# Optimization experiments

Measured on AMD Instinct MI355X. Metric: run time of the kernel, lower is better.

The kernel has to match this reference:

```python
import jax, jax.numpy as jnp
import numpy as np

NUM_CLASSES = 2
THRESHOLD = 0.35
NEGPOS_RATIO = 7
VARIANCES = (0.1, 0.2)
B, P, O = 64, 16800, 64  # batch, num_priors, num_objs per image


def point_form(pr):
    # cxcywh -> xyxy
    return jnp.concatenate([pr[:, :2] - pr[:, 2:] / 2, pr[:, :2] + pr[:, 2:] / 2], axis=1)


def jaccard(a, b):
    # a: [A,4] xyxy, b: [Bx,4] xyxy -> IoU [A,Bx]
    lt = jnp.maximum(a[:, None, :2], b[None, :, :2])
    rb = jnp.minimum(a[:, None, 2:], b[None, :, 2:])
    wh = jnp.clip(rb - lt, 0.0)
    inter = wh[..., 0] * wh[..., 1]
    area_a = ((a[:, 2] - a[:, 0]) * (a[:, 3] - a[:, 1]))[:, None]
    area_b = ((b[:, 2] - b[:, 0]) * (b[:, 3] - b[:, 1]))[None, :]
    return inter / (area_a + area_b - inter)


def encode(matched, priors):
    # matched xyxy [P,4], priors cxcywh [P,4]
    g_cxcy = (matched[:, :2] + matched[:, 2:]) / 2 - priors[:, :2]
    g_cxcy = g_cxcy / (VARIANCES[0] * priors[:, 2:])
    g_wh = (matched[:, 2:] - matched[:, :2]) / priors[:, 2:]
    g_wh = jnp.log(g_wh) / VARIANCES[1]
    return jnp.concatenate([g_cxcy, g_wh], axis=1)


def encode_landm(matched, priors):
    # matched [P,10] -> [P,5,2]
    m = matched.reshape(-1, 5, 2)
    g = (m - priors[:, None, :2]) / (VARIANCES[0] * priors[:, None, 2:])
    return g.reshape(-1, 10)


def match_one(truths, labels, landms, priors):
    # truths [O,4], labels [O], landms [O,10]
    overlaps = jaccard(truths, point_form(priors))  # [O,P]
    best_prior_overlap = overlaps.max(axis=1)       # per-gt best IoU
    best_prior_idx = overlaps.argmax(axis=1)
    valid_gt = best_prior_overlap >= 0.2
    best_truth_overlap = overlaps.max(axis=0)       # per-prior best IoU
    best_truth_idx = overlaps.argmax(axis=0)
    # index_fill(2) only for valid gts (best_prior_idx_filter)
    bto = best_truth_overlap.at[best_prior_idx].set(
        jnp.where(valid_gt, 2.0, best_truth_overlap[best_prior_idx]))
    # ensure every gt keeps its best prior
    bti = best_truth_idx.at[best_prior_idx].set(jnp.arange(truths.shape[0]))
    matches = truths[bti]                  # [P,4]
    conf = labels[bti]                     # [P]
    conf = jnp.where(bto < THRESHOLD, 0.0, conf)
    loc = encode(matches, priors)
    landm = encode_landm(landms[bti], priors)
    return loc, conf, landm


def smooth_l1_sum(x, mask):
    ax = jnp.abs(x)
    v = jnp.where(ax < 1.0, 0.5 * ax * ax, ax - 0.5)
    return (v * mask).sum()


def setup_inputs() -> dict:
    key = jax.random.key(0)
    k1, k2, k3, k4, k5, k6, k7, k8 = jax.random.split(key, 8)
    loc_data = jax.random.normal(k1, (B, P, 4), jnp.float32)
    conf_data = jax.random.normal(k2, (B, P, NUM_CLASSES), jnp.float32)
    landm_data = jax.random.normal(k3, (B, P, 10), jnp.float32)
    # priors: cx,cy in (0,1), w,h in (0.02,0.22)
    cxy = jax.random.uniform(k4, (P, 2), jnp.float32)
    wh = jax.random.uniform(k5, (P, 2), jnp.float32) * 0.2 + 0.02
    priors = jnp.concatenate([cxy, wh], axis=1)
    # targets: valid corner boxes + landmarks + label in {1,-1}
    xy1 = jax.random.uniform(k6, (B, O, 2), jnp.float32) * 0.6
    bwh = jax.random.uniform(k7, (B, O, 2), jnp.float32) * 0.3 + 0.05
    boxes = jnp.concatenate([xy1, xy1 + bwh], axis=-1)
    lms = jax.random.uniform(k8, (B, O, 10), jnp.float32)
    lab = jnp.where(jax.random.uniform(jax.random.fold_in(key, 9), (B, O, 1)) < 0.3, -1.0, 1.0)
    targets = jnp.concatenate([boxes, lms, lab], axis=-1)
    return {"loc_data": loc_data, "conf_data": conf_data, "landm_data": landm_data,
            "priors": priors, "targets": targets}


def reference(loc_data, conf_data, landm_data, priors, targets):
    num = loc_data.shape[0]
    num_priors = priors.shape[0]
    truths = targets[:, :, :4]
    landms = targets[:, :, 4:14]
    labels = targets[:, :, -1]
    loc_t, conf_t, landm_t = jax.vmap(match_one, in_axes=(0, 0, 0, None))(
        truths, labels, landms, priors)  # [B,P,4], [B,P], [B,P,10]

    # landmark loss over conf_t > 0
    pos1 = conf_t > 0
    num_pos_landm = pos1.astype(jnp.int32).sum(axis=1, keepdims=True)
    N1 = jnp.maximum(num_pos_landm.sum().astype(jnp.float32), 1.0)
    loss_landm = smooth_l1_sum(landm_data - landm_t, pos1[..., None].astype(landm_data.dtype))

    # localization loss over conf_t != 0 ; conf_t[pos] = 1
    pos = conf_t != 0
    conf_t01 = jnp.where(pos, 1, 0)  # int {0,1}
    loss_l = smooth_l1_sum(loc_data - loc_t, pos[..., None].astype(loc_data.dtype))

    # hard negative mining on per-prior CE loss (global-max log_sum_exp, as in source)
    batch_conf = conf_data.reshape(-1, NUM_CLASSES)
    x_max = batch_conf.max()
    lse = jnp.log(jnp.exp(batch_conf - x_max).sum(axis=1, keepdims=True)) + x_max
    gathered = jnp.take_along_axis(batch_conf, conf_t01.reshape(-1, 1), axis=1)
    loss_c = (lse - gathered).reshape(num, -1)  # [B,P]; positives NOT zeroed (as in source)
    loss_idx = jnp.argsort(-loss_c, axis=1)
    idx_rank = jnp.argsort(loss_idx, axis=1)
    num_pos = pos.astype(jnp.int32).sum(axis=1, keepdims=True)  # [B,1]
    num_neg = jnp.minimum(NEGPOS_RATIO * num_pos, num_priors - 1)
    neg = idx_rank < num_neg  # [B,P]
    neg_pos = pos | neg

    # cross-entropy (sum) over selected pos+neg priors
    logp = jax.nn.log_softmax(conf_data, axis=-1)  # [B,P,C]
    ce = -jnp.take_along_axis(logp, conf_t01[..., None], axis=-1)[..., 0]
    loss_c_final = (ce * neg_pos.astype(ce.dtype)).sum()

    N = jnp.maximum(num_pos.sum().astype(jnp.float32), 1.0)
    return (loss_l / N, loss_c_final / N, loss_landm / N1)
```

## Files before the change

kernel.cpp:

```cpp
#include <hip/hip_runtime.h>
#include <math.h>

#define BN 64
#define PN 16800
#define ON 64
#define THRESH 0.35f
#define NEGPOS 7
#define GX 66
#define NBLK (BN * GX)
#define NBP 1024
#define NCELL 256
#define NCB 66
#define EPSW 0.0009765625f
#define IOUF 0.3499f
#define TAILT 104

__device__ __forceinline__ unsigned f2key(float f) {
  unsigned u = __float_as_uint(f);
  return (u & 0x80000000u) ? ~u : (u | 0x80000000u);
}
__device__ __forceinline__ float key2f(unsigned k) {
  unsigned u = (k & 0x80000000u) ? (k & 0x7FFFFFFFu) : ~k;
  return __uint_as_float(u);
}
__device__ __forceinline__ float sl1(float d) {
  float a = fabsf(d);
  return (a < 1.f) ? 0.5f * a * a : a - 0.5f;
}

__global__ void k_count(const float* __restrict__ priors,
                        unsigned char* __restrict__ pcell,
                        unsigned* __restrict__ gcnt,
                        unsigned* __restrict__ gmax) {
  __shared__ unsigned lcnt[NCELL];
  int tid = threadIdx.x;
  lcnt[tid] = 0;
  __syncthreads();
  int p = blockIdx.x * 256 + tid;
  float mw = 0.f, mh = 0.f;
  if (p < PN) {
    float4 pr = reinterpret_cast<const float4*>(priors)[p];
    int cx = (int)(pr.x * 16.f); cx = cx < 0 ? 0 : (cx > 15 ? 15 : cx);
    int cy = (int)(pr.y * 16.f); cy = cy < 0 ? 0 : (cy > 15 ? 15 : cy);
    int cell = cy * 16 + cx;
    pcell[p] = (unsigned char)cell;
    atomicAdd(&lcnt[cell], 1u);
    mw = pr.z * 0.5f;
    mh = pr.w * 0.5f;
  }
#pragma unroll
  for (int off = 32; off; off >>= 1) {
    mw = fmaxf(mw, __shfl_xor(mw, off));
    mh = fmaxf(mh, __shfl_xor(mh, off));
  }
  if ((tid & 63) == 0) {
    atomicMax(&gmax[0], __float_as_uint(mw));
    atomicMax(&gmax[1], __float_as_uint(mh));
  }
  __syncthreads();
  unsigned c = lcnt[tid];
  if (c) atomicAdd(&gcnt[tid], c);
}

__global__ void k_scatter(const float* __restrict__ priors,
                          const float* __restrict__ targets,
                          const unsigned char* __restrict__ pcell,
                          const unsigned* __restrict__ gcnt,
                          unsigned* __restrict__ gcur,
                          const unsigned* __restrict__ gmax,
                          float4* __restrict__ sbox,
                          int* __restrict__ sorig,
                          int* __restrict__ cellOff,
                          unsigned long long* __restrict__ tmask) {
  int bid = blockIdx.x;
  int tid = threadIdx.x;
  if (bid < NCB) {
    __shared__ unsigned tmp[NCELL];
    __shared__ unsigned excl[NCELL];
    __shared__ unsigned lcnt[NCELL];
    __shared__ unsigned lbase[NCELL];
    unsigned c = gcnt[tid];
    tmp[tid] = c;
    lcnt[tid] = 0;
    __syncthreads();
    for (int off = 1; off < NCELL; off <<= 1) {
      unsigned v = (tid >= off) ? tmp[tid - off] : 0u;
      __syncthreads();
      tmp[tid] += v;
      __syncthreads();
    }
    excl[tid] = tmp[tid] - c;
    if (bid == 0) {
      cellOff[tid] = (int)(tmp[tid] - c);
      if (tid == 0) cellOff[NCELL] = PN;
    }
    __syncthreads();
    int p = bid * 256 + tid;
    bool valid = p < PN;
    int cell = 0; unsigned lrank = 0;
    if (valid) {
      cell = pcell[p];
      lrank = atomicAdd(&lcnt[cell], 1u);
    }
    __syncthreads();
    if (lcnt[tid]) lbase[tid] = atomicAdd(&gcur[tid], lcnt[tid]);
    __syncthreads();
    if (valid) {
      int slot = (int)(excl[cell] + lbase[cell] + lrank);
      float4 pr = reinterpret_cast<const float4*>(priors)[p];
      float px1 = pr.x - pr.z * 0.5f, py1 = pr.y - pr.w * 0.5f;
      float px2 = pr.x + pr.z * 0.5f, py2 = pr.y + pr.w * 0.5f;
      sbox[slot] = make_float4(px1, py1, px2, py2);
      sorig[slot] = p;
    }
  } else {
    int b = bid - NCB;
    __shared__ float4 tb[ON];
    if (tid < ON) {
      const float* tg = &targets[((long)b * ON + tid) * 15];
      tb[tid] = make_float4(tg[0], tg[1], tg[2], tg[3]);
    }
    __syncthreads();
    float MW = __uint_as_float(gmax[0]), MH = __uint_as_float(gmax[1]);
    int cx = tid & 15, cy = tid >> 4;
    float cxl = (float)cx * 0.0625f, cxh = (float)(cx + 1) * 0.0625f;
    float cyl = (float)cy * 0.0625f, cyh = (float)(cy + 1) * 0.0625f;
    float pmaxa = 4.f * MW * MH;
    unsigned long long m = 0ull;
    for (int t = 0; t < ON; t++) {
      float4 a = tb[t];
      float wt = a.z - a.x, ht = a.w - a.y;
      float at = wt * ht;
      float need = IOUF * at;
      float wmin = need / fminf(ht, 2.f * MH);
      float hmin = need / fminf(wt, 2.f * MW);
      float wx0 = a.x + wmin - MW - EPSW, wx1 = a.z - wmin + MW + EPSW;
      float wy0 = a.y + hmin - MH - EPSW, wy1 = a.w - hmin + MH + EPSW;
      bool ok = (pmaxa >= need) &&
                (cxh > wx0) && (cxl < wx1) &&
                (cyh > wy0) && (cyl < wy1);
      if (ok) m |= (1ull << t);
    }
    tmask[b * NCELL + tid] = m;
  }
}

__global__ void k_bp(const float* __restrict__ targets,
                     const float4* __restrict__ sbox,
                     const int* __restrict__ sorig,
                     const int* __restrict__ cellOff,
                     const unsigned* __restrict__ gmax,
                     unsigned long long* __restrict__ bpp) {
  int bid = blockIdx.x;
  int tid = threadIdx.x;
  int lane = tid & 63, wv = tid >> 6;
  int b = bid >> 4;
  int t = ((bid & 15) << 2) + wv;
  const float* tg = &targets[((long)b * ON + t) * 15];
  float ax1 = tg[0], ay1 = tg[1], ax2 = tg[2], ay2 = tg[3];
  float aa = (ax2 - ax1) * (ay2 - ay1);
  float MW = __uint_as_float(gmax[0]), MH = __uint_as_float(gmax[1]);
  int xlo = (int)floorf((ax1 - MW - EPSW) * 16.f); xlo = xlo < 0 ? 0 : (xlo > 15 ? 15 : xlo);
  int xhi = (int)floorf((ax2 + MW + EPSW) * 16.f); xhi = xhi < 0 ? 0 : (xhi > 15 ? 15 : xhi);
  int ylo = (int)floorf((ay1 - MH - EPSW) * 16.f); ylo = ylo < 0 ? 0 : (ylo > 15 ? 15 : ylo);
  int yhi = (int)floorf((ay2 + MH + EPSW) * 16.f); yhi = yhi < 0 ? 0 : (yhi > 15 ? 15 : yhi);
  float bi = 0.f, bu = 1.f; int bp = 0;
  for (int cy = ylo; cy <= yhi; cy++) {
    int s0 = cellOff[cy * 16 + xlo];
    int s1 = cellOff[cy * 16 + xhi + 1];
    for (int s = s0 + lane; s < s1; s += 64) {
      float4 pr = sbox[s];
      int op = sorig[s];
      float ab2 = (pr.z - pr.x) * (pr.w - pr.y);
      float lx = fmaxf(ax1, pr.x), ly = fmaxf(ay1, pr.y);
      float rx = fminf(ax2, pr.z), ry = fminf(ay2, pr.w);
      float w = fmaxf(rx - lx, 0.f), h = fmaxf(ry - ly, 0.f);
      float inter = w * h;
      float uni = aa + ab2 - inter;
      float A = inter * bu, C = bi * uni;
      if (A > C || (A == C && op < bp)) { bi = inter; bu = uni; bp = op; }
    }
  }
#pragma unroll
  for (int off = 1; off < 64; off <<= 1) {
    float oi = __shfl_xor(bi, off), ou = __shfl_xor(bu, off);
    int op = __shfl_xor(bp, off);
    float A = oi * bu, C = bi * ou;
    if (A > C || (A == C && op < bp)) { bi = oi; bu = ou; bp = op; }
  }
  if (lane == 0) {
    float q = bi / bu;
    bpp[(long)b * ON + t] = ((unsigned long long)f2key(q) << 32) | (unsigned)(~bp);
  }
}

__global__ void k_encode(const float* __restrict__ loc_data,
                         const float* __restrict__ conf_data,
                         const float* __restrict__ landm_data,
                         const float* __restrict__ priors,
                         const float* __restrict__ targets,
                         const unsigned char* __restrict__ pcell,
                         const unsigned long long* __restrict__ tmask,
                         const unsigned long long* __restrict__ bpp,
                         float* __restrict__ lossc, unsigned char* __restrict__ posf,
                         float* __restrict__ part_l, float* __restrict__ part_lm,
                         int* __restrict__ np_part, int* __restrict__ np1_part) {
  int b = blockIdx.y;
  int p = blockIdx.x * 256 + threadIdx.x;
  int bid = b * GX + blockIdx.x;
  __shared__ float4 tgs4[ON * 15 / 4];
  __shared__ float4 tb[ON];
  __shared__ float ta[ON];
  __shared__ unsigned long long smask[NCELL];
  __shared__ int ovr[256];
  float* tgs = (float*)tgs4;
  if (threadIdx.x < ON * 15 / 4)
    tgs4[threadIdx.x] = reinterpret_cast<const float4*>(targets + (long)b * ON * 15)[threadIdx.x];
  smask[threadIdx.x] = tmask[b * NCELL + threadIdx.x];
  if (threadIdx.x < ON) {
    const float* tg = &targets[((long)b * ON + threadIdx.x) * 15];
    float4 bx = make_float4(tg[0], tg[1], tg[2], tg[3]);
    tb[threadIdx.x] = bx;
    ta[threadIdx.x] = (bx.z - bx.x) * (bx.w - bx.y);
  }
  ovr[threadIdx.x] = -1;
  __syncthreads();
  if (threadIdx.x < ON) {
    int t = threadIdx.x;
    unsigned long long best = bpp[(long)b * ON + t];
    float q = key2f((unsigned)(best >> 32));
    int qp = (int)(~(unsigned)best);
    int s0 = blockIdx.x * 256;
    if (qp >= s0 && qp < s0 + 256) {
      int valid = (q >= 0.2f) ? 1 : 0;
      atomicMax(&ovr[qp - s0], (t << 1) | valid);
    }
  }
  __syncthreads();

  float sum_l = 0.f, sum_lm = 0.f;
  int cp = 0, cp1 = 0;
  if (p < PN) {
    float4 pr = reinterpret_cast<const float4*>(priors)[p];
    float px1 = pr.x - pr.z * 0.5f, py1 = pr.y - pr.w * 0.5f;
    float px2 = pr.x + pr.z * 0.5f, py2 = pr.y + pr.w * 0.5f;
    float ab2 = (px2 - px1) * (py2 - py1);
    unsigned long long m = smask[pcell[p]];
    float bi = 0.f, bu = 1.f; int t = 0;
    while (m) {
      int t0 = __builtin_ctzll(m); m &= m - 1;
      float4 a0 = tb[t0];
      float lx = fmaxf(a0.x, px1), ly = fmaxf(a0.y, py1);
      float rx = fminf(a0.z, px2), ry = fminf(a0.w, py2);
      float w2 = fmaxf(rx - lx, 0.f), h2 = fmaxf(ry - ly, 0.f);
      float inter = w2 * h2;
      float uni = ta[t0] + ab2 - inter;
      if (inter * bu > bi * uni) { bi = inter; bu = uni; t = t0; }
    }
    bool pos = (bi / bu) >= THRESH;
    int o = ovr[threadIdx.x];
    if (o >= 0) { t = o >> 1; if (o & 1) pos = true; }
    const float* tg = &tgs[t * 15];
    float label = tg[14];
    bool pos1 = pos && (label > 0.f);
    if (pos) {
      float rz = 1.0f / pr.z, rw = 1.0f / pr.w;
      float m0 = tg[0], m1 = tg[1], m2 = tg[2], m3 = tg[3];
      float g0 = ((m0 + m2) * 0.5f - pr.x) * rz * 10.f;
      float g1 = ((m1 + m3) * 0.5f - pr.y) * rw * 10.f;
      float g2 = __logf((m2 - m0) * rz) * 5.f;
      float g3 = __logf((m3 - m1) * rw) * 5.f;
      const float* ld = &loc_data[((long)b * PN + p) * 4];
      sum_l = sl1(ld[0] - g0) + sl1(ld[1] - g1) + sl1(ld[2] - g2) + sl1(ld[3] - g3);
      cp = 1;
      if (pos1) {
        const float* lm = &landm_data[((long)b * PN + p) * 10];
#pragma unroll
        for (int i = 0; i < 5; i++) {
          float gx = (tg[4 + 2 * i] - pr.x) * rz * 10.f;
          float gy = (tg[5 + 2 * i] - pr.y) * rw * 10.f;
          sum_lm += sl1(lm[2 * i] - gx) + sl1(lm[2 * i + 1] - gy);
        }
        cp1 = 1;
      }
    }
    float2 c2 = reinterpret_cast<const float2*>(conf_data)[(long)b * PN + p];
    float mx = fmaxf(c2.x, c2.y);
    float lse = mx + __logf(__expf(c2.x - mx) + __expf(c2.y - mx));
    lossc[b * PN + p] = lse - (pos ? c2.y : c2.x);
    posf[b * PN + p] = pos ? 1 : 0;
  }
  for (int off = 32; off; off >>= 1) {
    sum_l += __shfl_down(sum_l, off);
    sum_lm += __shfl_down(sum_lm, off);
    cp += __shfl_down(cp, off);
    cp1 += __shfl_down(cp1, off);
  }
  __shared__ float sl4[4], slm4[4];
  __shared__ int sp4[4], sp14[4];
  int w = threadIdx.x >> 6;
  if ((threadIdx.x & 63) == 0) { sl4[w] = sum_l; slm4[w] = sum_lm; sp4[w] = cp; sp14[w] = cp1; }
  __syncthreads();
  if (threadIdx.x == 0) {
    part_l[bid] = sl4[0] + sl4[1] + sl4[2] + sl4[3];
    part_lm[bid] = slm4[0] + slm4[1] + slm4[2] + slm4[3];
    np_part[bid] = sp4[0] + sp4[1] + sp4[2] + sp4[3];
    np1_part[bid] = sp14[0] + sp14[1] + sp14[2] + sp14[3];
  }
}

__global__ void __launch_bounds__(1024) k_select(const float* __restrict__ lossc,
                                                 const unsigned char* __restrict__ posf,
                                                 const int* __restrict__ np_part,
                                                 const int* __restrict__ np1_part,
                                                 const float* __restrict__ part_l,
                                                 const float* __restrict__ part_lm,
                                                 float* __restrict__ rout) {
  int b = blockIdx.x;
  int tid = threadIdx.x;
  int lane = tid & 63;
  int wv = tid >> 6;
  __shared__ int s_np, s_rnp1;
  __shared__ float s_rsl, s_rslm;
  __shared__ unsigned s_lo, s_hi, s_cg, s_totp;
  __shared__ unsigned fcnt[16];
  __shared__ unsigned wsc[16];
  __shared__ float wsum[16];
  const float* row = &lossc[(long)b * PN];
  const unsigned char* prow = &posf[(long)b * PN];

  if (tid == 0) {
    s_np = 0; s_rnp1 = 0; s_rsl = 0.f; s_rslm = 0.f;
    s_lo = 0u; s_hi = 0xFFFFFFFFu;
  }
  __syncthreads();
  if (tid < GX) {
    atomicAdd(&s_np, np_part[b * GX + tid]);
    atomicAdd(&s_rsl, part_l[b * GX + tid]);
    atomicAdd(&s_rslm, part_lm[b * GX + tid]);
    atomicAdd(&s_rnp1, np1_part[b * GX + tid]);
  }

  const float4* rf4 = reinterpret_cast<const float4*>(row);
  const uint4* pw4 = reinterpret_cast<const uint4*>(prow);
  bool hasTail = tid < TAILT;
  float vm[16];
  float vt[4];
  {
    float4 L0 = rf4[tid * 4], L1 = rf4[tid * 4 + 1], L2 = rf4[tid * 4 + 2], L3 = rf4[tid * 4 + 3];
    vm[0] = L0.x; vm[1] = L0.y; vm[2] = L0.z; vm[3] = L0.w;
    vm[4] = L1.x; vm[5] = L1.y; vm[6] = L1.z; vm[7] = L1.w;
    vm[8] = L2.x; vm[9] = L2.y; vm[10] = L2.z; vm[11] = L2.w;
    vm[12] = L3.x; vm[13] = L3.y; vm[14] = L3.z; vm[15] = L3.w;
  }
  unsigned pmask = 0;
  {
    uint4 W = pw4[tid];
    unsigned w0 = W.x, w1 = W.y, w2 = W.z, w3 = W.w;
#pragma unroll
    for (int j = 0; j < 4; j++) {
      pmask |= ((w0 >> (8 * j)) & 1u) << j;
      pmask |= ((w1 >> (8 * j)) & 1u) << (4 + j);
      pmask |= ((w2 >> (8 * j)) & 1u) << (8 + j);
      pmask |= ((w3 >> (8 * j)) & 1u) << (12 + j);
    }
  }
  unsigned tmask = 0;
  if (hasTail) {
    float4 Lt = rf4[4096 + tid];
    vt[0] = Lt.x; vt[1] = Lt.y; vt[2] = Lt.z; vt[3] = Lt.w;
    unsigned Wt = reinterpret_cast<const unsigned*>(prow)[4096 + tid];
#pragma unroll
    for (int j = 0; j < 4; j++) tmask |= ((Wt >> (8 * j)) & 1u) << j;
  } else {
    vt[0] = vt[1] = vt[2] = vt[3] = -1.f;
  }
  unsigned km[16], kt4[4];
#pragma unroll
  for (int j = 0; j < 16; j++) km[j] = f2key(vm[j]);
#pragma unroll
  for (int j = 0; j < 4; j++) kt4[j] = f2key(vt[j]);
  __syncthreads();
  int np = s_np;
  int k = NEGPOS * np;
  if (k > PN - 1) k = PN - 1;
  bool haveNeg = (k > 0);

  unsigned T = 0, Rsel = 0;
  if (haveNeg) {
    for (int it = 0; it < 32; it++) {
      unsigned lo = s_lo, hi = s_hi;
      unsigned mid = lo + ((hi - lo) >> 1) + ((hi - lo) & 1u);
      unsigned c = 0;
#pragma unroll
      for (int j = 0; j < 16; j++) c += (km[j] >= mid) ? 1u : 0u;
      if (hasTail) {
#pragma unroll
        for (int j = 0; j < 4; j++) c += (kt4[j] >= mid) ? 1u : 0u;
      }
#pragma unroll
      for (int o = 32; o; o >>= 1) c += (unsigned)__shfl_down((int)c, o);
      if (lane == 0) fcnt[wv] = c;
      __syncthreads();
      if (tid == 0) {
        unsigned tot = 0;
        for (int i = 0; i < 16; i++) tot += fcnt[i];
        if (tot >= (unsigned)k) s_lo = mid; else s_hi = mid - 1;
      }
      __syncthreads();
      if (s_lo >= s_hi) break;
    }
    T = s_lo;
    unsigned c = 0;
#pragma unroll
    for (int j = 0; j < 16; j++) c += (km[j] > T) ? 1u : 0u;
    if (hasTail) {
#pragma unroll
      for (int j = 0; j < 4; j++) c += (kt4[j] > T) ? 1u : 0u;
    }
#pragma unroll
    for (int o = 32; o; o >>= 1) c += (unsigned)__shfl_down((int)c, o);
    if (lane == 0) fcnt[wv] = c;
    __syncthreads();
    if (tid == 0) {
      unsigned tot = 0;
      for (int i = 0; i < 16; i++) tot += fcnt[i];
      s_cg = tot;
    }
    __syncthreads();
    Rsel = (unsigned)k - s_cg;
  }

  unsigned mc = 0, tc = 0;
  if (haveNeg) {
#pragma unroll
    for (int j = 0; j < 16; j++) mc += (km[j] == T) ? 1u : 0u;
    if (hasTail) {
#pragma unroll
      for (int j = 0; j < 4; j++) tc += (kt4[j] == T) ? 1u : 0u;
    }
  }
  unsigned packed = mc | (tc << 16);
  unsigned inc = packed;
#pragma unroll
  for (int o = 1; o < 64; o <<= 1) {
    unsigned u = (unsigned)__shfl_up((int)inc, o);
    if (lane >= o) inc += u;
  }
  if (lane == 63) wsc[wv] = inc;
  __syncthreads();
  if (tid == 0) {
    unsigned run = 0;
    for (int i = 0; i < 16; i++) { unsigned t2 = wsc[i]; wsc[i] = run; run += t2; }
    s_totp = run;
  }
  __syncthreads();
  unsigned excl = wsc[wv] + inc - packed;
  unsigned mb = excl & 0xFFFFu;
  unsigned tb2 = (s_totp & 0xFFFFu) + (excl >> 16);

  float acc = 0.f;
  unsigned cm = 0;
#pragma unroll
  for (int j = 0; j < 16; j++) {
    float v2 = vm[j];
    bool pos = (pmask >> j) & 1u;
    if (pos) acc += v2;
    if (haveNeg) {
      if (km[j] > T) { if (!pos) acc += v2; }
      else if (km[j] == T) {
        unsigned r2 = mb + cm; cm++;
        if (!pos && r2 < Rsel) acc += v2;
      }
    }
  }
  if (hasTail) {
    unsigned ct = 0;
#pragma unroll
    for (int j = 0; j < 4; j++) {
      float v2 = vt[j];
      bool pos = (tmask >> j) & 1u;
      if (pos) acc += v2;
      if (haveNeg) {
        if (kt4[j] > T) { if (!pos) acc += v2; }
        else if (kt4[j] == T) {
          unsigned r2 = tb2 + ct; ct++;
          if (!pos && r2 < Rsel) acc += v2;
        }
      }
    }
  }
#pragma unroll
  for (int o = 32; o; o >>= 1) acc += __shfl_down(acc, o);
  if (lane == 0) wsum[wv] = acc;
  __syncthreads();
  if (tid == 0) {
    float tot = 0.f;
    for (int i = 0; i < 16; i++) tot += wsum[i];
    rout[b * 8 + 0] = tot;
    rout[b * 8 + 1] = s_rsl;
    rout[b * 8 + 2] = s_rslm;
    ((int*)rout)[b * 8 + 3] = np;
    ((int*)rout)[b * 8 + 4] = s_rnp1;
  }
}

__global__ void k_final(const float* __restrict__ rout, float* __restrict__ out) {
  int tid = threadIdx.x;
  float sc = rout[tid * 8 + 0];
  float sl = rout[tid * 8 + 1];
  float slm = rout[tid * 8 + 2];
  int np = ((const int*)rout)[tid * 8 + 3];
  int np1 = ((const int*)rout)[tid * 8 + 4];
#pragma unroll
  for (int o = 32; o; o >>= 1) {
    sc += __shfl_down(sc, o);
    sl += __shfl_down(sl, o);
    slm += __shfl_down(slm, o);
    np += __shfl_down(np, o);
    np1 += __shfl_down(np1, o);
  }
  if (tid == 0) {
    float N = fmaxf((float)np, 1.f);
    float N1 = fmaxf((float)np1, 1.f);
    out[0] = sl / N;
    out[1] = sc / N;
    out[2] = slm / N1;
  }
}

extern "C" void kernel_launch(void* const* d_in, const int* in_sizes, int n_in,
                              void* d_out, int out_size, void* d_ws, size_t ws_size,
                              hipStream_t stream) {
  const float* loc_data = (const float*)d_in[0];
  const float* conf_data = (const float*)d_in[1];
  const float* landm_data = (const float*)d_in[2];
  const float* priors = (const float*)d_in[3];
  const float* targets = (const float*)d_in[4];
  float* out = (float*)d_out;

  char* ws = (char*)d_ws;
  size_t off = 0;
  float* lossc = (float*)(ws + off); off += (size_t)BN * PN * 4;
  unsigned char* posf = (unsigned char*)(ws + off); off += (size_t)BN * PN;
  off = (off + 15) & ~(size_t)15;
  unsigned long long* bpp = (unsigned long long*)(ws + off); off += (size_t)BN * ON * 8;
  float* part_l = (float*)(ws + off); off += NBLK * 4;
  float* part_lm = (float*)(ws + off); off += NBLK * 4;
  int* np_part = (int*)(ws + off); off += NBLK * 4;
  int* np1_part = (int*)(ws + off); off += NBLK * 4;
  float4* sbox = (float4*)(ws + off); off += (size_t)PN * 16;
  int* sorig = (int*)(ws + off); off += (size_t)PN * 4;
  unsigned char* pcell = (unsigned char*)(ws + off); off += (size_t)PN;
  off = (off + 15) & ~(size_t)15;
  int* cellOff = (int*)(ws + off); off += 260 * 4;
  unsigned long long* tmask = (unsigned long long*)(ws + off); off += (size_t)BN * NCELL * 8;
  off = (off + 15) & ~(size_t)15;
  float* rout = (float*)(ws + off); off += (size_t)BN * 8 * 4;
  off = (off + 15) & ~(size_t)15;
  unsigned* zreg = (unsigned*)(ws + off);
  unsigned* gcnt = zreg;
  unsigned* gcur = zreg + 256;
  unsigned* gmax = zreg + 512;
  size_t zbytes = (256 + 256 + 4) * 4;
  off += zbytes;

  hipMemsetAsync(zreg, 0, zbytes, stream);
  k_count<<<NCB, 256, 0, stream>>>(priors, pcell, gcnt, gmax);
  k_scatter<<<NCB + BN, 256, 0, stream>>>(priors, targets, pcell, gcnt, gcur, gmax,
                                          sbox, sorig, cellOff, tmask);
  k_bp<<<NBP, 256, 0, stream>>>(targets, sbox, sorig, cellOff, gmax, bpp);
  dim3 gbp(GX, BN);
  k_encode<<<gbp, 256, 0, stream>>>(loc_data, conf_data, landm_data, priors, targets,
                                    pcell, tmask, bpp, lossc, posf,
                                    part_l, part_lm, np_part, np1_part);
  k_select<<<BN, 1024, 0, stream>>>(lossc, posf, np_part, np1_part, part_l, part_lm,
                                    rout);
  k_final<<<1, 64, 0, stream>>>(rout, out);
}
```

Measured before the change: 212.1 us.

## Drop memset and final kernel via per-block histograms and last-block reduction

Replaces the global atomic cell counts and max with per-block histograms and per-block maxima, so the prefix scan is computed deterministically from all block histograms and the memset launch goes away. The final reduction kernel is folded into k_select with global atomics and a last-block ticket. The IoU loop in k_encode is also unrolled to process two candidate targets per iteration for more ILP. This trades two launches for redundant histogram reads in every scatter block and atomic float accumulation, which makes the order of summation nondeterministic.

Result: slower. 224.5 us (+5.8%).

```diff
diff --git a/kernel.cpp b/kernel.cpp
--- a/kernel.cpp
+++ b/kernel.cpp
@@ -15,6 +15,13 @@
 #define IOUF 0.3499f
 #define TAILT 104
 
+struct GAcc {
+  unsigned ticket;
+  float sl, slm, sc;
+  int np, np1;
+  unsigned pad0, pad1;
+};
+
 __device__ __forceinline__ unsigned f2key(float f) {
   unsigned u = __float_as_uint(f);
   return (u & 0x80000000u) ? ~u : (u | 0x80000000u);
@@ -30,13 +37,17 @@
 
 __global__ void k_count(const float* __restrict__ priors,
                         unsigned char* __restrict__ pcell,
-                        unsigned* __restrict__ gcnt,
-                        unsigned* __restrict__ gmax) {
+                        unsigned* __restrict__ bhist,
+                        float* __restrict__ gmaxblk,
+                        GAcc* __restrict__ gacc) {
   __shared__ unsigned lcnt[NCELL];
+  __shared__ float swm[4], swh[4];
   int tid = threadIdx.x;
+  int bid = blockIdx.x;
   lcnt[tid] = 0;
-  __syncthreads();
-  int p = blockIdx.x * 256 + tid;
+  if (bid == 0 && tid < 8) ((unsigned*)gacc)[tid] = 0;
+  __syncthreads();
+  int p = bid * 256 + tid;
   float mw = 0.f, mh = 0.f;
   if (p < PN) {
     float4 pr = reinterpret_cast<const float4*>(priors)[p];
@@ -53,21 +64,21 @@
     mw = fmaxf(mw, __shfl_xor(mw, off));
     mh = fmaxf(mh, __shfl_xor(mh, off));
   }
-  if ((tid & 63) == 0) {
-    atomicMax(&gmax[0], __float_as_uint(mw));
-    atomicMax(&gmax[1], __float_as_uint(mh));
-  }
-  __syncthreads();
-  unsigned c = lcnt[tid];
-  if (c) atomicAdd(&gcnt[tid], c);
+  if ((tid & 63) == 0) { swm[tid >> 6] = mw; swh[tid >> 6] = mh; }
+  __syncthreads();
+  if (tid == 0) {
+    gmaxblk[bid * 2] = fmaxf(fmaxf(swm[0], swm[1]), fmaxf(swm[2], swm[3]));
+    gmaxblk[bid * 2 + 1] = fmaxf(fmaxf(swh[0], swh[1]), fmaxf(swh[2], swh[3]));
+  }
+  bhist[bid * NCELL + tid] = lcnt[tid];
 }
 
 __global__ void k_scatter(const float* __restrict__ priors,
                           const float* __restrict__ targets,
                           const unsigned char* __restrict__ pcell,
-                          const unsigned* __restrict__ gcnt,
-                          unsigned* __restrict__ gcur,
-                          const unsigned* __restrict__ gmax,
+                          const unsigned* __restrict__ bhist,
+                          const float* __restrict__ gmaxblk,
+                          unsigned* __restrict__ gmax,
                           float4* __restrict__ sbox,
                           int* __restrict__ sorig,
                           int* __restrict__ cellOff,
@@ -76,11 +87,16 @@
   int tid = threadIdx.x;
   if (bid < NCB) {
     __shared__ unsigned tmp[NCELL];
-    __shared__ unsigned excl[NCELL];
+    __shared__ unsigned sbase[NCELL];
     __shared__ unsigned lcnt[NCELL];
-    __shared__ unsigned lbase[NCELL];
-    unsigned c = gcnt[tid];
-    tmp[tid] = c;
+    unsigned tot = 0, mybase = 0;
+#pragma unroll 4
+    for (int b2 = 0; b2 < NCB; b2++) {
+      unsigned h = bhist[b2 * NCELL + tid];
+      if (b2 < bid) mybase += h;
+      tot += h;
+    }
+    tmp[tid] = tot;
     lcnt[tid] = 0;
     __syncthreads();
     for (int off = 1; off < NCELL; off <<= 1) {
@@ -89,24 +105,27 @@
       tmp[tid] += v;
       __syncthreads();
     }
-    excl[tid] = tmp[tid] - c;
+    unsigned excl = tmp[tid] - tot;
+    sbase[tid] = excl + mybase;
     if (bid == 0) {
-      cellOff[tid] = (int)(tmp[tid] - c);
-      if (tid == 0) cellOff[NCELL] = PN;
+      cellOff[tid] = (int)excl;
+      if (tid == 0) {
+        cellOff[NCELL] = PN;
+        float MW = 0.f, MH = 0.f;
+        for (int i = 0; i < NCB; i++) {
+          MW = fmaxf(MW, gmaxblk[2 * i]);
+          MH = fmaxf(MH, gmaxblk[2 * i + 1]);
+        }
+        gmax[0] = __float_as_uint(MW);
+        gmax[1] = __float_as_uint(MH);
+      }
     }
     __syncthreads();
     int p = bid * 256 + tid;
-    bool valid = p < PN;
-    int cell = 0; unsigned lrank = 0;
-    if (valid) {
-      cell = pcell[p];
-      lrank = atomicAdd(&lcnt[cell], 1u);
-    }
-    __syncthreads();
-    if (lcnt[tid]) lbase[tid] = atomicAdd(&gcur[tid], lcnt[tid]);
-    __syncthreads();
-    if (valid) {
-      int slot = (int)(excl[cell] + lbase[cell] + lrank);
+    if (p < PN) {
+      int cell = pcell[p];
+      unsigned lrank = atomicAdd(&lcnt[cell], 1u);
+      int slot = (int)(sbase[cell] + lrank);
       float4 pr = reinterpret_cast<const float4*>(priors)[p];
       float px1 = pr.x - pr.z * 0.5f, py1 = pr.y - pr.w * 0.5f;
       float px2 = pr.x + pr.z * 0.5f, py2 = pr.y + pr.w * 0.5f;
@@ -121,7 +140,11 @@
       tb[tid] = make_float4(tg[0], tg[1], tg[2], tg[3]);
     }
     __syncthreads();
-    float MW = __uint_as_float(gmax[0]), MH = __uint_as_float(gmax[1]);
+    float MW = 0.f, MH = 0.f;
+    for (int i = 0; i < NCB; i++) {
+      MW = fmaxf(MW, gmaxblk[2 * i]);
+      MH = fmaxf(MH, gmaxblk[2 * i + 1]);
+    }
     int cx = tid & 15, cy = tid >> 4;
     float cxl = (float)cx * 0.0625f, cxh = (float)(cx + 1) * 0.0625f;
     float cyl = (float)cy * 0.0625f, cyh = (float)(cy + 1) * 0.0625f;
@@ -249,13 +272,28 @@
     float bi = 0.f, bu = 1.f; int t = 0;
     while (m) {
       int t0 = __builtin_ctzll(m); m &= m - 1;
-      float4 a0 = tb[t0];
-      float lx = fmaxf(a0.x, px1), ly = fmaxf(a0.y, py1);
-      float rx = fminf(a0.z, px2), ry = fminf(a0.w, py2);
-      float w2 = fmaxf(rx - lx, 0.f), h2 = fmaxf(ry - ly, 0.f);
-      float inter = w2 * h2;
-      float uni = ta[t0] + ab2 - inter;
-      if (inter * bu > bi * uni) { bi = inter; bu = uni; t = t0; }
+      float4 a0 = tb[t0]; float aa0 = ta[t0];
+      if (m) {
+        int t1 = __builtin_ctzll(m); m &= m - 1;
+        float4 a1 = tb[t1]; float aa1 = ta[t1];
+        float lx0 = fmaxf(a0.x, px1), ly0 = fmaxf(a0.y, py1);
+        float rx0 = fminf(a0.z, px2), ry0 = fminf(a0.w, py2);
+        float w0 = fmaxf(rx0 - lx0, 0.f), h0 = fmaxf(ry0 - ly0, 0.f);
+        float in0 = w0 * h0, un0 = aa0 + ab2 - in0;
+        float lx1 = fmaxf(a1.x, px1), ly1 = fmaxf(a1.y, py1);
+        float rx1 = fminf(a1.z, px2), ry1 = fminf(a1.w, py2);
+        float w1 = fmaxf(rx1 - lx1, 0.f), h1 = fmaxf(ry1 - ly1, 0.f);
+        float in1 = w1 * h1, un1 = aa1 + ab2 - in1;
+        if (in0 * bu > bi * un0) { bi = in0; bu = un0; t = t0; }
+        if (in1 * bu > bi * un1) { bi = in1; bu = un1; t = t1; }
+      } else {
+        float lx = fmaxf(a0.x, px1), ly = fmaxf(a0.y, py1);
+        float rx = fminf(a0.z, px2), ry = fminf(a0.w, py2);
+        float w2 = fmaxf(rx - lx, 0.f), h2 = fmaxf(ry - ly, 0.f);
+        float inter = w2 * h2;
+        float uni = aa0 + ab2 - inter;
+        if (inter * bu > bi * uni) { bi = inter; bu = uni; t = t0; }
+      }
     }
     bool pos = (bi / bu) >= THRESH;
     int o = ovr[threadIdx.x];
@@ -315,7 +353,8 @@
                                                  const int* __restrict__ np1_part,
                                                  const float* __restrict__ part_l,
                                                  const float* __restrict__ part_lm,
-                                                 float* __restrict__ rout) {
+                                                 GAcc* __restrict__ gacc,
+                                                 float* __restrict__ out) {
   int b = blockIdx.x;
   int tid = threadIdx.x;
   int lane = tid & 63;
@@ -494,35 +533,29 @@
   for (int o = 32; o; o >>= 1) acc += __shfl_down(acc, o);
   if (lane == 0) wsum[wv] = acc;
   __syncthreads();
+
   if (tid == 0) {
     float tot = 0.f;
     for (int i = 0; i < 16; i++) tot += wsum[i];
-    rout[b * 8 + 0] = tot;
-    rout[b * 8 + 1] = s_rsl;
-    rout[b * 8 + 2] = s_rslm;
-    ((int*)rout)[b * 8 + 3] = np;
-    ((int*)rout)[b * 8 + 4] = s_rnp1;
-  }
-}
-
-__global__ void k_final(const float* __restrict__ rout, float* __restrict__ out) {
-  int tid = threadIdx.x;
-  float sc = rout[tid * 8 + 0];
-  float sl = rout[tid * 8 + 1];
-  float slm = rout[tid * 8 + 2];
-  int np = ((const int*)rout)[tid * 8 + 3];
-  int np1 = ((const int*)rout)[tid * 8 + 4];
-#pragma unroll
-  for (int o = 32; o; o >>= 1) {
-    sc += __shfl_down(sc, o);
-    sl += __shfl_down(sl, o);
-    slm += __shfl_down(slm, o);
-    np += __shfl_down(np, o);
-    np1 += __shfl_down(np1, o);
-  }
-  if (tid == 0) {
-    float N = fmaxf((float)np, 1.f);
-    float N1 = fmaxf((float)np1, 1.f);
+    atomicAdd(&gacc->sc, tot);
+    atomicAdd(&gacc->sl, s_rsl);
+    atomicAdd(&gacc->slm, s_rslm);
+    atomicAdd(&gacc->np, np);
+    atomicAdd(&gacc->np1, s_rnp1);
+  }
+  __threadfence();
+  __shared__ int lastF;
+  if (tid == 0) lastF = (atomicAdd(&gacc->ticket, 1u) == (unsigned)(BN - 1)) ? 1 : 0;
+  __syncthreads();
+  if (lastF && tid == 0) {
+    __threadfence();
+    float sl = atomicAdd(&gacc->sl, 0.f);
+    float slm = atomicAdd(&gacc->slm, 0.f);
+    float sc = atomicAdd(&gacc->sc, 0.f);
+    int tnp = atomicAdd(&gacc->np, 0);
+    int tnp1 = atomicAdd(&gacc->np1, 0);
+    float N = fmaxf((float)tnp, 1.f);
+    float N1 = fmaxf((float)tnp1, 1.f);
     out[0] = sl / N;
     out[1] = sc / N;
     out[2] = slm / N1;
@@ -556,18 +589,13 @@
   int* cellOff = (int*)(ws + off); off += 260 * 4;
   unsigned long long* tmask = (unsigned long long*)(ws + off); off += (size_t)BN * NCELL * 8;
   off = (off + 15) & ~(size_t)15;
-  float* rout = (float*)(ws + off); off += (size_t)BN * 8 * 4;
-  off = (off + 15) & ~(size_t)15;
-  unsigned* zreg = (unsigned*)(ws + off);
-  unsigned* gcnt = zreg;
-  unsigned* gcur = zreg + 256;
-  unsigned* gmax = zreg + 512;
-  size_t zbytes = (256 + 256 + 4) * 4;
-  off += zbytes;
-
-  hipMemsetAsync(zreg, 0, zbytes, stream);
-  k_count<<<NCB, 256, 0, stream>>>(priors, pcell, gcnt, gmax);
-  k_scatter<<<NCB + BN, 256, 0, stream>>>(priors, targets, pcell, gcnt, gcur, gmax,
+  unsigned* bhist = (unsigned*)(ws + off); off += (size_t)NCB * NCELL * 4;
+  float* gmaxblk = (float*)(ws + off); off += (size_t)NCB * 2 * 4;
+  unsigned* gmax = (unsigned*)(ws + off); off += 16;
+  GAcc* gacc = (GAcc*)(ws + off); off += sizeof(GAcc);
+
+  k_count<<<NCB, 256, 0, stream>>>(priors, pcell, bhist, gmaxblk, gacc);
+  k_scatter<<<NCB + BN, 256, 0, stream>>>(priors, targets, pcell, bhist, gmaxblk, gmax,
                                           sbox, sorig, cellOff, tmask);
   k_bp<<<NBP, 256, 0, stream>>>(targets, sbox, sorig, cellOff, gmax, bpp);
   dim3 gbp(GX, BN);
@@ -575,6 +603,5 @@
                                     pcell, tmask, bpp, lossc, posf,
                                     part_l, part_lm, np_part, np1_part);
   k_select<<<BN, 1024, 0, stream>>>(lossc, posf, np_part, np1_part, part_l, part_lm,
-                                    rout);
-  k_final<<<1, 64, 0, stream>>>(rout, out);
-}
+                                    gacc, out);
+}
```
